# Performance work log

Hardware: AMD Instinct MI355X
Metric: run time of the kernel (lower is better)

The kernel has to match this reference:

```python
import jax, jax.numpy as jnp
import numpy as np


def setup_inputs() -> dict:
    key = jax.random.key(0)
    ks = jax.random.split(key, 8)
    B, S, D, H = 32, 8192, 256, 256  # batch, seq_len, input_dim, hidden_dim
    bound = 1.0 / np.sqrt(H)
    x = jax.random.normal(ks[0], (B, H), dtype=jnp.float32)
    context = jax.random.normal(ks[1], (B, S, D), dtype=jnp.float32)
    mask = jax.random.randint(ks[2], (B, S), 0, 2, dtype=jnp.int32)
    # input_linear: Linear(H, H)
    W_in = jax.random.uniform(ks[3], (H, H), jnp.float32, -bound, bound)
    b_in = jax.random.uniform(ks[4], (H,), jnp.float32, -bound, bound)
    # context_linear: Conv1d(D, H, kernel=1) == pointwise linear over features
    W_ctx = jax.random.uniform(ks[5], (H, D), jnp.float32, -1.0 / np.sqrt(D), 1.0 / np.sqrt(D))
    b_ctx = jax.random.uniform(ks[6], (H,), jnp.float32, -1.0 / np.sqrt(D), 1.0 / np.sqrt(D))
    V = jax.random.uniform(ks[7], (H,), jnp.float32, -bound, bound)
    return {"x": x, "context": context, "mask": mask,
            "W_in": W_in, "b_in": b_in, "W_ctx": W_ctx, "b_ctx": b_ctx, "V": V}


def reference(x, context, mask, W_in, b_in, W_ctx, b_ctx, V):
    # inp: [B, H] -> broadcast over seq as [B, 1, H]
    inp = (x @ W_in.T + b_in)[:, None, :]
    # ctx: Conv1d(kernel=1) over permuted context == per-position linear: [B, S, H]
    ctx = jnp.einsum('bsd,hd->bsh', context, W_ctx) + b_ctx
    # score: V . tanh(inp + ctx) reduced over H -> [B, S]
    att = jnp.einsum('bsh,h->bs', jnp.tanh(inp + ctx), V)
    att = 10.0 * jnp.tanh(att)
    att = jnp.where(mask.astype(bool), att, -jnp.inf)
    ans = jax.nn.softmax(att, axis=1)
    indices = jnp.argmax(ans, axis=1)
    p = jnp.max(ans, axis=1)
    return (indices, p[:, None], mask.astype(bool))
```

## Files before the change

### kernel.cpp

```cpp
#include <hip/hip_runtime.h>
#include <math.h>

#define S_LEN 8192
#define BATCH 32
#define HDIM 256
#define DDIM 256
#define SCHUNK 1024
#define NSUB 16
#define TSUB 64
#define LDK 264

typedef float f32x4 __attribute__((ext_vector_type(4)));
typedef __fp16 h16x2 __attribute__((ext_vector_type(2)));
typedef __fp16 h16x4 __attribute__((ext_vector_type(4)));
typedef _Float16 f16x8 __attribute__((ext_vector_type(8)));

static __device__ __forceinline__ float fast_tanh(float x) {
    float e = __expf(2.0f * x);
    return 1.0f - 2.0f / (e + 1.0f);
}

static __device__ __forceinline__ void cvt_store(f32x4 v, _Float16* ph, _Float16* pl) {
    h16x2 h0 = __builtin_amdgcn_cvt_pkrtz(v[0], v[1]);
    h16x2 h1 = __builtin_amdgcn_cvt_pkrtz(v[2], v[3]);
    h16x2 l0 = __builtin_amdgcn_cvt_pkrtz(v[0] - (float)h0[0], v[1] - (float)h0[1]);
    h16x2 l1 = __builtin_amdgcn_cvt_pkrtz(v[2] - (float)h1[0], v[3] - (float)h1[1]);
    h16x4 hi; hi[0] = h0[0]; hi[1] = h0[1]; hi[2] = h1[0]; hi[3] = h1[1];
    h16x4 lo; lo[0] = l0[0]; lo[1] = l0[1]; lo[2] = l1[0]; lo[3] = l1[1];
    *(h16x4*)ph = hi;
    *(h16x4*)pl = lo;
}

__global__ void prep_kernel(const float* __restrict__ x,
                            const float* __restrict__ W_in,
                            const float* __restrict__ b_in,
                            const float* __restrict__ W_ctx,
                            const float* __restrict__ b_ctx,
                            float* __restrict__ cin,
                            _Float16* __restrict__ Wf,
                            unsigned long long* __restrict__ pmax,
                            float* __restrict__ psum,
                            int* __restrict__ pcnt) {
    __shared__ float xs[DDIM];
    const int bx = blockIdx.x;
    const int t  = threadIdx.x;
    if (bx < BATCH) {
        if (t == 0) {
            pmax[bx] = 0ull;
            psum[bx] = 0.0f;
            pcnt[bx] = 0;
        }
        xs[t] = x[bx * DDIM + t];
        __syncthreads();
        const float* wr = W_in + t * DDIM;
        float acc = b_in[t] + b_ctx[t];
        #pragma unroll 8
        for (int d = 0; d < DDIM; ++d) acc += xs[d] * wr[d];
        cin[bx * HDIM + t] = acc;
    } else {
        const int g  = (bx - BATCH) * 256 + t;
        const int ht = g >> 9;
        const int ks = (g >> 6) & 7;
        const int l  = g & 63;
        const int h  = ht * 16 + (l & 15);
        const int d0 = ks * 32 + (l >> 4) * 8;
        const float* src = W_ctx + h * DDIM + d0;
        f16x8 vh;
        #pragma unroll
        for (int j = 0; j < 8; ++j) vh[j] = (_Float16)src[j];
        *(f16x8*)(Wf + (size_t)g * 8) = vh;
    }
}

__launch_bounds__(512, 2)
__global__ void att_kernel(const float* __restrict__ context,
                           const int* __restrict__ mask,
                           const float* __restrict__ cin,
                           const float* __restrict__ V,
                           const _Float16* __restrict__ Wf,
                           float* __restrict__ out,
                           float* __restrict__ out_mask,
                           unsigned long long* __restrict__ pmax,
                           float* __restrict__ psum,
                           int* __restrict__ pcnt) {
    __shared__ __align__(16) _Float16 a_hi[2][TSUB * LDK];
    __shared__ __align__(16) _Float16 a_lo[2][TSUB * LDK];
    __shared__ float att_part[2][8][TSUB];

    const int schunk = blockIdx.x;
    const int b      = blockIdx.y;
    const int t      = threadIdx.x;
    const int w      = t >> 6;
    const int l      = t & 63;
    const int lane16 = l & 15;
    const int q      = l >> 4;

    f16x8 wfrag[2][8];
    #pragma unroll
    for (int ht = 0; ht < 2; ++ht)
        #pragma unroll
        for (int ks = 0; ks < 8; ++ks)
            wfrag[ht][ks] = *(const f16x8*)(Wf + (size_t)(((w * 2 + ht) * 8 + ks) * 64 + l) * 8);

    f32x4 cinr4[2], vr4[2];
    #pragma unroll
    for (int ht = 0; ht < 2; ++ht)
        #pragma unroll
        for (int r = 0; r < 4; ++r) {
            int h = (w * 2 + ht) * 16 + q * 4 + r;
            cinr4[ht][r] = cin[b * HDIM + h];
            vr4[ht][r]   = V[h];
        }

    const float* cbase = context + ((size_t)b * S_LEN + (size_t)schunk * SCHUNK) * DDIM;

    float best = -INFINITY;
    int   bid  = 0x7fffffff;
    float sume = 0.0f;

    #pragma unroll
    for (int i = 0; i < 8; ++i) {
        int f = i * 512 + t, row = f >> 6, c4 = f & 63;
        f32x4 v = *(const f32x4*)(cbase + row * DDIM + c4 * 4);
        cvt_store(v, &a_hi[0][row * LDK + c4 * 4], &a_lo[0][row * LDK + c4 * 4]);
    }
    __syncthreads();

    for (int it = 0; it < NSUB; ++it) {
        const int cur = it & 1;
        const bool pre = (it + 1 < NSUB);

        f32x4 pf[8];
        if (pre) {
            const float* nb = cbase + (size_t)(it + 1) * TSUB * DDIM;
            #pragma unroll
            for (int i = 0; i < 8; ++i) {
                int f = i * 512 + t, row = f >> 6, c4 = f & 63;
                pf[i] = *(const f32x4*)(nb + row * DDIM + c4 * 4);
            }
        }

        f32x4 acc[2][4];
        #pragma unroll
        for (int ht = 0; ht < 2; ++ht)
            #pragma unroll
            for (int nt = 0; nt < 4; ++nt) acc[ht][nt] = cinr4[ht];
        #pragma unroll
        for (int ks = 0; ks < 8; ++ks) {
            #pragma unroll
            for (int nt = 0; nt < 4; ++nt) {
                int o = (nt * 16 + lane16) * LDK + ks * 32 + q * 8;
                f16x8 bh = *(const f16x8*)(&a_hi[cur][o]);
                f16x8 bl = *(const f16x8*)(&a_lo[cur][o]);
                #pragma unroll
                for (int ht = 0; ht < 2; ++ht) {
                    acc[ht][nt] = __builtin_amdgcn_mfma_f32_16x16x32_f16(wfrag[ht][ks], bh, acc[ht][nt], 0, 0, 0);
                    acc[ht][nt] = __builtin_amdgcn_mfma_f32_16x16x32_f16(wfrag[ht][ks], bl, acc[ht][nt], 0, 0, 0);
                }
            }
        }

        #pragma unroll
        for (int nt = 0; nt < 4; ++nt) {
            float p = 0.f;
            #pragma unroll
            for (int ht = 0; ht < 2; ++ht)
                #pragma unroll
                for (int r = 0; r < 4; ++r)
                    p += fast_tanh(acc[ht][nt][r]) * vr4[ht][r];
            p += __shfl_xor(p, 16);
            p += __shfl_xor(p, 32);
            if (l < 16) att_part[cur][w][nt * 16 + l] = p;
        }

        if (pre) {
            #pragma unroll
            for (int i = 0; i < 8; ++i) {
                int f = i * 512 + t, row = f >> 6, c4 = f & 63;
                cvt_store(pf[i], &a_hi[cur ^ 1][row * LDK + c4 * 4],
                                 &a_lo[cur ^ 1][row * LDK + c4 * 4]);
            }
        }
        __syncthreads();

        if (t < TSUB) {
            float a = 0.f;
            #pragma unroll
            for (int ww = 0; ww < 8; ++ww) a += att_part[cur][ww][t];
            a = 10.0f * fast_tanh(a);
            int s  = schunk * SCHUNK + it * TSUB + t;
            int mk = mask[b * S_LEN + s];
            out_mask[(size_t)b * S_LEN + s] = mk ? 1.0f : 0.0f;
            if (mk) {
                if (a > best) { best = a; bid = s; }
                sume += __expf(a - 10.0f);
            }
        }
    }

    if (w == 0) {
        #pragma unroll
        for (int off = 32; off > 0; off >>= 1) {
            float ov = __shfl_xor(best, off);
            int   oi = __shfl_xor(bid, off);
            float os = __shfl_xor(sume, off);
            sume += os;
            if (ov > best || (ov == best && oi < bid)) { best = ov; bid = oi; }
        }
        if (l == 0) {
            unsigned ub = __float_as_uint(best);
            ub = (ub & 0x80000000u) ? ~ub : (ub | 0x80000000u);
            unsigned long long pk =
                ((unsigned long long)ub << 32) | (unsigned long long)(0xFFFFFFFFu - (unsigned)bid);
            atomicMax(&pmax[b], pk);
            atomicAdd(&psum[b], sume);
            __threadfence();
            int old = atomicAdd(&pcnt[b], 1);
            if (old == 7) {
                __threadfence();
                unsigned long long m = atomicMax(&pmax[b], 0ull);
                float ssum = atomicAdd(&psum[b], 0.0f);
                unsigned mb = (unsigned)(m >> 32);
                float mv = (mb & 0x80000000u) ? __uint_as_float(mb ^ 0x80000000u)
                                              : __uint_as_float(~mb);
                int idx = (int)(0xFFFFFFFFu - (unsigned)(m & 0xFFFFFFFFull));
                out[b]         = (float)idx;
                out[BATCH + b] = __expf(mv - 10.0f) / ssum;
            }
        }
    }
}

extern "C" void kernel_launch(void* const* d_in, const int* in_sizes, int n_in,
                              void* d_out, int out_size, void* d_ws, size_t ws_size,
                              hipStream_t stream) {
    const float* x       = (const float*)d_in[0];
    const float* context = (const float*)d_in[1];
    const int*   mask    = (const int*)d_in[2];
    const float* W_in    = (const float*)d_in[3];
    const float* b_in    = (const float*)d_in[4];
    const float* W_ctx   = (const float*)d_in[5];
    const float* b_ctx   = (const float*)d_in[6];
    const float* V       = (const float*)d_in[7];
    float* out = (float*)d_out;

    char* ws = (char*)d_ws;
    float*              cin  = (float*)ws;
    _Float16*           Wf   = (_Float16*)(ws + 32 * 1024);
    unsigned long long* pmax = (unsigned long long*)(ws + 160 * 1024);
    float*              psum = (float*)(ws + 160 * 1024 + 256);
    int*                pcnt = (int*)(ws + 160 * 1024 + 384);

    float* out_mask = out + 64;

    prep_kernel<<<64, 256, 0, stream>>>(x, W_in, b_in, W_ctx, b_ctx, cin, Wf,
                                        pmax, psum, pcnt);
    dim3 grid(S_LEN / SCHUNK, BATCH);
    att_kernel<<<grid, 512, 0, stream>>>(context, mask, cin, V, Wf,
                                         out, out_mask, pmax, psum, pcnt);
}
```

Measured before the change: 394.8 us.

## Fuse prep work into attention kernel and replace atomics with slot-based final reduction

The separate prep kernel is removed. Each attention block now computes its batch's input projection in shared memory and converts W_ctx fragments to fp16 directly from global memory, overlapping this with the first context tile load. The atomic max/add cross-block reduction with a completion counter is replaced by per-block result slots written to workspace plus a tiny final kernel that reduces them. This removes one launch's dependency and the atomics, but every one of the 256 blocks now redundantly does a 256x256 matvec and fp32-to-fp16 weight conversion, and a second launch is added at the end.

```diff
diff --git a/kernel.cpp b/kernel.cpp
--- a/kernel.cpp
+++ b/kernel.cpp
@@ -31,61 +31,22 @@
     *(h16x4*)pl = lo;
 }
 
-__global__ void prep_kernel(const float* __restrict__ x,
-                            const float* __restrict__ W_in,
-                            const float* __restrict__ b_in,
-                            const float* __restrict__ W_ctx,
-                            const float* __restrict__ b_ctx,
-                            float* __restrict__ cin,
-                            _Float16* __restrict__ Wf,
-                            unsigned long long* __restrict__ pmax,
-                            float* __restrict__ psum,
-                            int* __restrict__ pcnt) {
-    __shared__ float xs[DDIM];
-    const int bx = blockIdx.x;
-    const int t  = threadIdx.x;
-    if (bx < BATCH) {
-        if (t == 0) {
-            pmax[bx] = 0ull;
-            psum[bx] = 0.0f;
-            pcnt[bx] = 0;
-        }
-        xs[t] = x[bx * DDIM + t];
-        __syncthreads();
-        const float* wr = W_in + t * DDIM;
-        float acc = b_in[t] + b_ctx[t];
-        #pragma unroll 8
-        for (int d = 0; d < DDIM; ++d) acc += xs[d] * wr[d];
-        cin[bx * HDIM + t] = acc;
-    } else {
-        const int g  = (bx - BATCH) * 256 + t;
-        const int ht = g >> 9;
-        const int ks = (g >> 6) & 7;
-        const int l  = g & 63;
-        const int h  = ht * 16 + (l & 15);
-        const int d0 = ks * 32 + (l >> 4) * 8;
-        const float* src = W_ctx + h * DDIM + d0;
-        f16x8 vh;
-        #pragma unroll
-        for (int j = 0; j < 8; ++j) vh[j] = (_Float16)src[j];
-        *(f16x8*)(Wf + (size_t)g * 8) = vh;
-    }
-}
-
 __launch_bounds__(512, 2)
 __global__ void att_kernel(const float* __restrict__ context,
                            const int* __restrict__ mask,
-                           const float* __restrict__ cin,
                            const float* __restrict__ V,
-                           const _Float16* __restrict__ Wf,
-                           float* __restrict__ out,
+                           const float* __restrict__ W_in,
+                           const float* __restrict__ b_in,
+                           const float* __restrict__ W_ctx,
+                           const float* __restrict__ b_ctx,
+                           const float* __restrict__ x,
                            float* __restrict__ out_mask,
-                           unsigned long long* __restrict__ pmax,
-                           float* __restrict__ psum,
-                           int* __restrict__ pcnt) {
+                           f32x4* __restrict__ slots) {
     __shared__ __align__(16) _Float16 a_hi[2][TSUB * LDK];
     __shared__ __align__(16) _Float16 a_lo[2][TSUB * LDK];
     __shared__ float att_part[2][8][TSUB];
+    __shared__ float xs[DDIM];
+    __shared__ float cin_s[HDIM];
 
     const int schunk = blockIdx.x;
     const int b      = blockIdx.y;
@@ -95,12 +56,46 @@
     const int lane16 = l & 15;
     const int q      = l >> 4;
 
+    const float* cbase = context + ((size_t)b * S_LEN + (size_t)schunk * SCHUNK) * DDIM;
+
+    f32x4 st0[8];
+    #pragma unroll
+    for (int i = 0; i < 8; ++i) {
+        int f = i * 512 + t, row = f >> 6, c4 = f & 63;
+        st0[i] = *(const f32x4*)(cbase + row * DDIM + c4 * 4);
+    }
+    if (t < DDIM) xs[t] = x[b * DDIM + t];
+
     f16x8 wfrag[2][8];
     #pragma unroll
     for (int ht = 0; ht < 2; ++ht)
         #pragma unroll
-        for (int ks = 0; ks < 8; ++ks)
-            wfrag[ht][ks] = *(const f16x8*)(Wf + (size_t)(((w * 2 + ht) * 8 + ks) * 64 + l) * 8);
+        for (int ks = 0; ks < 8; ++ks) {
+            const float* wsrc = W_ctx + (size_t)((w * 2 + ht) * 16 + lane16) * DDIM
+                              + ks * 32 + q * 8;
+            f32x4 w0 = *(const f32x4*)wsrc;
+            f32x4 w1 = *(const f32x4*)(wsrc + 4);
+            f16x8 vh;
+            #pragma unroll
+            for (int j = 0; j < 4; ++j) { vh[j] = (_Float16)w0[j]; vh[4 + j] = (_Float16)w1[j]; }
+            wfrag[ht][ks] = vh;
+        }
+
+    #pragma unroll
+    for (int i = 0; i < 8; ++i) {
+        int f = i * 512 + t, row = f >> 6, c4 = f & 63;
+        cvt_store(st0[i], &a_hi[0][row * LDK + c4 * 4], &a_lo[0][row * LDK + c4 * 4]);
+    }
+    __syncthreads();
+
+    if (t < HDIM) {
+        const float* wr = W_in + t * DDIM;
+        float acc = b_in[t] + b_ctx[t];
+        #pragma unroll 8
+        for (int d = 0; d < DDIM; ++d) acc += xs[d] * wr[d];
+        cin_s[t] = acc;
+    }
+    __syncthreads();
 
     f32x4 cinr4[2], vr4[2];
     #pragma unroll
@@ -108,23 +103,13 @@
         #pragma unroll
         for (int r = 0; r < 4; ++r) {
             int h = (w * 2 + ht) * 16 + q * 4 + r;
-            cinr4[ht][r] = cin[b * HDIM + h];
+            cinr4[ht][r] = cin_s[h];
             vr4[ht][r]   = V[h];
         }
-
-    const float* cbase = context + ((size_t)b * S_LEN + (size_t)schunk * SCHUNK) * DDIM;
 
     float best = -INFINITY;
     int   bid  = 0x7fffffff;
     float sume = 0.0f;
-
-    #pragma unroll
-    for (int i = 0; i < 8; ++i) {
-        int f = i * 512 + t, row = f >> 6, c4 = f & 63;
-        f32x4 v = *(const f32x4*)(cbase + row * DDIM + c4 * 4);
-        cvt_store(v, &a_hi[0][row * LDK + c4 * 4], &a_lo[0][row * LDK + c4 * 4]);
-    }
-    __syncthreads();
 
     for (int it = 0; it < NSUB; ++it) {
         const int cur = it & 1;
@@ -208,26 +193,36 @@
             if (ov > best || (ov == best && oi < bid)) { best = ov; bid = oi; }
         }
         if (l == 0) {
-            unsigned ub = __float_as_uint(best);
-            ub = (ub & 0x80000000u) ? ~ub : (ub | 0x80000000u);
-            unsigned long long pk =
-                ((unsigned long long)ub << 32) | (unsigned long long)(0xFFFFFFFFu - (unsigned)bid);
-            atomicMax(&pmax[b], pk);
-            atomicAdd(&psum[b], sume);
-            __threadfence();
-            int old = atomicAdd(&pcnt[b], 1);
-            if (old == 7) {
-                __threadfence();
-                unsigned long long m = atomicMax(&pmax[b], 0ull);
-                float ssum = atomicAdd(&psum[b], 0.0f);
-                unsigned mb = (unsigned)(m >> 32);
-                float mv = (mb & 0x80000000u) ? __uint_as_float(mb ^ 0x80000000u)
-                                              : __uint_as_float(~mb);
-                int idx = (int)(0xFFFFFFFFu - (unsigned)(m & 0xFFFFFFFFull));
-                out[b]         = (float)idx;
-                out[BATCH + b] = __expf(mv - 10.0f) / ssum;
-            }
-        }
+            f32x4 sl;
+            sl[0] = best;
+            sl[1] = __int_as_float(bid);
+            sl[2] = sume;
+            sl[3] = 0.0f;
+            slots[b * 8 + schunk] = sl;
+        }
+    }
+}
+
+__global__ void final_kernel(const f32x4* __restrict__ slots,
+                             float* __restrict__ out) {
+    const int t  = threadIdx.x;
+    const int b  = t >> 3;
+    const int ln = t & 7;
+    f32x4 sl = slots[b * 8 + ln];
+    float fb = sl[0];
+    int   fi = __float_as_int(sl[1]);
+    float fs = sl[2];
+    #pragma unroll
+    for (int off = 1; off < 8; off <<= 1) {
+        float ov = __shfl_xor(fb, off);
+        int   oi = __shfl_xor(fi, off);
+        float os = __shfl_xor(fs, off);
+        fs += os;
+        if (ov > fb || (ov == fb && oi < fi)) { fb = ov; fi = oi; }
+    }
+    if (ln == 0) {
+        out[b]         = (float)fi;
+        out[BATCH + b] = __expf(fb - 10.0f) / fs;
     }
 }
 
@@ -244,18 +239,11 @@
     const float* V       = (const float*)d_in[7];
     float* out = (float*)d_out;
 
-    char* ws = (char*)d_ws;
-    float*              cin  = (float*)ws;
-    _Float16*           Wf   = (_Float16*)(ws + 32 * 1024);
-    unsigned long long* pmax = (unsigned long long*)(ws + 160 * 1024);
-    float*              psum = (float*)(ws + 160 * 1024 + 256);
-    int*                pcnt = (int*)(ws + 160 * 1024 + 384);
-
+    f32x4* slots    = (f32x4*)d_ws;
     float* out_mask = out + 64;
 
-    prep_kernel<<<64, 256, 0, stream>>>(x, W_in, b_in, W_ctx, b_ctx, cin, Wf,
-                                        pmax, psum, pcnt);
     dim3 grid(S_LEN / SCHUNK, BATCH);
-    att_kernel<<<grid, 512, 0, stream>>>(context, mask, cin, V, Wf,
-                                         out, out_mask, pmax, psum, pcnt);
-}
+    att_kernel<<<grid, 512, 0, stream>>>(context, mask, V, W_in, b_in,
+                                         W_ctx, b_ctx, x, out_mask, slots);
+    final_kernel<<<1, 256, 0, stream>>>(slots, out);
+}
```

Measured after the change: 399.5 us. Within noise of the previous version (+1.2%).
